# Performance work log

Hardware: AMD Instinct MI355X
Metric: run time of the kernel (lower is better)

The kernel has to match this reference:

```python
import jax, jax.numpy as jnp
import numpy as np

HID = 192
EPS = 1e-5

def _bn(x, g, b):
    # BatchNorm1d, training mode: batch stats over all leading axes, biased var
    ax = tuple(range(x.ndim - 1))
    m = x.mean(axis=ax)
    v = x.var(axis=ax)
    return (x - m) * jax.lax.rsqrt(v + EPS) * g + b

def _glorot(k, shape):
    lim = np.sqrt(6.0 / (shape[0] + shape[1]))
    return jax.random.uniform(k, shape, jnp.float32, -lim, lim)

def setup_inputs() -> dict:
    key = jax.random.key(0)
    ks = jax.random.split(key, 8)
    B, N, F, C = 16, 1024, 128, 10
    x = jax.random.normal(ks[0], (B, N, F), jnp.float32)
    adj = (jax.random.uniform(ks[1], (B, N, N)) < 0.01).astype(jnp.float32)
    adj = jnp.maximum(adj, jnp.swapaxes(adj, 1, 2))
    return dict(
        x=x, adj=adj,
        bn_feat_g=jnp.ones((F,), jnp.float32), bn_feat_b=jnp.full((F,), 1e-4, jnp.float32),
        W_feat=_glorot(ks[2], (F, HID)),
        bns_conv_g=jnp.ones((3, HID), jnp.float32), bns_conv_b=jnp.full((3, HID), 1e-4, jnp.float32),
        convs_W=jnp.stack([_glorot(jax.random.fold_in(ks[3], i), (HID, HID)) for i in range(3)]),
        convs_b=jnp.zeros((3, HID), jnp.float32),
        bn_fc_g=jnp.ones((HID,), jnp.float32), bn_fc_b=jnp.full((HID,), 1e-4, jnp.float32),
        lin_W=_glorot(ks[4], (HID, HID)), lin_b=jnp.zeros((HID,), jnp.float32),
        bn_hid_g=jnp.ones((HID,), jnp.float32), bn_hid_b=jnp.full((HID,), 1e-4, jnp.float32),
        cls_W=_glorot(ks[5], (HID, 10)), cls_b=jnp.zeros((10,), jnp.float32),
    )

def reference(x, adj, bn_feat_g, bn_feat_b, W_feat, bns_conv_g, bns_conv_b,
              convs_W, convs_b, bn_fc_g, bn_fc_b, lin_W, lin_b,
              bn_hid_g, bn_hid_b, cls_W, cls_b):
    B, N, _ = x.shape
    # dense_to_sparse discards edge values -> binary edges; add remaining self loops (weight 1)
    A = (adj != 0).astype(x.dtype)
    A = jnp.maximum(A, jnp.eye(N, dtype=x.dtype))
    deg = A.sum(-1)                                   # [B,N]
    dis = jnp.where(deg > 0, deg ** -0.5, 0.0)
    A_hat = dis[:, :, None] * A * dis[:, None, :]      # D^-1/2 (A+I) D^-1/2
    h = _bn(x, bn_feat_g, bn_feat_b)
    # conv_feat has gfn=True: pure linear transform, no bias, no propagation
    h = jax.nn.relu(jnp.einsum('bnf,fh->bnh', h, W_feat))
    for i in range(convs_W.shape[0]):
        h = _bn(h, bns_conv_g[i], bns_conv_b[i])
        h = jax.nn.relu(jnp.einsum('bij,bjh->bih', A_hat, h @ convs_W[i]) + convs_b[i])
    g = h.mean(axis=1)                                 # global_mean_pool -> [B,HID]
    g = _bn(g, bn_fc_g, bn_fc_b)
    g = jax.nn.relu(g @ lin_W + lin_b)
    g = _bn(g, bn_hid_g, bn_hid_b)
    logits = g @ cls_W + cls_b
    return jax.nn.log_softmax(logits, axis=-1)
```

## Files before the change

### kernel.cpp

```cpp
#include <hip/hip_runtime.h>
#include <hip/hip_bf16.h>

#define BB 16
#define NN 1024
#define FF 128
#define HH 192
#define NROWS (BB*NN)
#define MAXC 128
#define EPSV 1e-5f

constexpr size_t OFF_H0  = 0;
constexpr size_t OFF_ZB  = OFF_H0 + (size_t)NROWS*HH/2;
constexpr size_t OFF_WPF = OFF_ZB + (size_t)NROWS*HH/2;
constexpr size_t OFF_WPC = OFF_WPF + (size_t)HH*FF/2;
constexpr size_t OFF_BF  = OFF_WPC + (size_t)HH*HH/2;
constexpr size_t OFF_BC  = OFF_BF + HH;
constexpr size_t OFF_DIS = OFF_BC + HH;
constexpr size_t OFF_G   = OFF_DIS + NROWS;
constexpr size_t OFF_ST  = OFF_G + BB*HH;
constexpr size_t ST_SIZE = 512 + 3*8*512;
constexpr size_t OFF_FLAG= OFF_ST + ST_SIZE;
constexpr size_t OFF_CNT = OFF_FLAG + 1;
constexpr size_t OFF_COLS= OFF_CNT + NROWS;

typedef __attribute__((ext_vector_type(8))) short short8;
typedef __attribute__((ext_vector_type(4))) float f32x4;
typedef __attribute__((ext_vector_type(4))) unsigned int u32x4;
typedef __attribute__((ext_vector_type(2))) unsigned int u32x2;

static __device__ __forceinline__ float bf(const __hip_bfloat16 v) {
    return __bfloat162float(v);
}
static __device__ __forceinline__ float ldin(const void* p, size_t i, int isf) {
    return isf ? ((const float*)p)[i]
               : __bfloat162float(((const __hip_bfloat16*)p)[i]);
}
static __host__ __device__ __forceinline__ float* stage_h(float* ws, int s ) {
    return ws + OFF_ST + 512 + (size_t)s*8*512;
}
static __device__ __forceinline__ float blo(unsigned int u) {
    union { unsigned int x; float f; } v; v.x = u << 16; return v.f;
}
static __device__ __forceinline__ float bhi(unsigned int u) {
    union { unsigned int x; float f; } v; v.x = u & 0xFFFF0000u; return v.f;
}
static __device__ __forceinline__ unsigned int packbf(float a, float b) {
    union { unsigned int u; __hip_bfloat16 h[2]; } p;
    p.h[0] = __float2bfloat16(a); p.h[1] = __float2bfloat16(b);
    return p.u;
}

__global__ void detect_and_zero(const unsigned int* __restrict__ adjw, float* ws) {
    __shared__ int evid;
    int tid = threadIdx.x;
    if (tid == 0) evid = 0;
    __syncthreads();
    int local = 0;
    for (int k = tid; k < 16384; k += 256) {
        unsigned int w = adjw[k];
        if ((w & 0xFFFFu) == 0x3F80u) local++;
    }
    if (local) atomicAdd(&evid, local);
    for (size_t k = tid; k < ST_SIZE; k += 256) ws[OFF_ST + k] = 0.f;
    for (int k = tid; k < BB*HH; k += 256) ws[OFF_G + k] = 0.f;
    __syncthreads();
    if (tid == 0) ((int*)ws)[OFF_FLAG] = (evid == 0) ? 1 : 0;
}

__global__ __launch_bounds__(256) void phase1(const void* __restrict__ adj,
                                              const void* __restrict__ x, float* ws) {
    const int isf = ((const int*)ws)[OFF_FLAG];
    int tid = threadIdx.x;
    if (blockIdx.x < NROWS) {
        int row = blockIdx.x;
        int i   = row & (NN - 1);
        __shared__ int cnt_s;
        __shared__ unsigned short colbuf[MAXC];
        if (tid == 0) cnt_s = 0;
        __syncthreads();
        int j0 = tid*4;
        unsigned int bits[4];
        if (isf) {
            u32x4 v = *(const u32x4*)((const unsigned int*)adj + (size_t)row*NN + j0);
            bits[0]=v[0]; bits[1]=v[1]; bits[2]=v[2]; bits[3]=v[3];
        } else {
            u32x2 v = *(const u32x2*)((const unsigned short*)adj + (size_t)row*NN + j0);
            bits[0]=(v[0]&0xFFFFu); bits[1]=(v[0]>>16); bits[2]=(v[1]&0xFFFFu); bits[3]=(v[1]>>16);
        }
        #pragma unroll
        for (int e = 0; e < 4; ++e) {
            int j = j0 + e;
            if ((bits[e] << 1) != 0u || j == i) {
                int p = atomicAdd(&cnt_s, 1);
                if (p < MAXC) colbuf[p] = (unsigned short)j;
            }
        }
        __syncthreads();
        int c = cnt_s; if (c > MAXC) c = MAXC;
        if (tid == 0) {
            ((int*)(ws + OFF_CNT))[row] = c;
            ws[OFF_DIS + row] = rsqrtf((float)cnt_s);
        }
        unsigned short* cols = (unsigned short*)(ws + OFF_COLS);
        for (int k = tid; k < c; k += 256) cols[(size_t)row*MAXC + k] = colbuf[k];
    } else {
        int b2 = blockIdx.x - NROWS;
        int f = tid & (FF-1), half = tid >> 7;
        int r0 = b2*64 + half*32;
        float s = 0.f, sq = 0.f;
        for (int r = 0; r < 32; ++r) {
            float v = ldin(x, (size_t)(r0 + r)*FF + f, isf);
            s += v; sq += v*v;
        }
        atomicAdd(&ws[OFF_ST + f], s);
        atomicAdd(&ws[OFF_ST + 256 + f], sq);
    }
}

__global__ void prep_feat(const void* __restrict__ W_feat,
                          const void* __restrict__ gg, const void* __restrict__ bb,
                          float* ws) {
    const int isf = ((const int*)ws)[OFF_FLAG];
    int n = blockIdx.x, k = threadIdx.x;
    const float* st = ws + OFF_ST;
    float m   = st[k] * (1.f/NROWS);
    float var = st[256+k] * (1.f/NROWS) - m*m;
    float a   = ldin(gg, k, isf) * rsqrtf(var + EPSV);
    float c   = ldin(bb, k, isf) - m*a;
    float wv  = ldin(W_feat, (size_t)k*HH + n, isf);
    ((__hip_bfloat16*)(ws + OFF_WPF))[(size_t)n*FF + k] = __float2bfloat16(a*wv);
    __shared__ float red[FF];
    red[k] = c*wv;
    __syncthreads();
    for (int s = FF/2; s > 0; s >>= 1) {
        if (k < s) red[k] += red[k + s];
        __syncthreads();
    }
    if (k == 0) ws[OFF_BF + n] = red[0];
}

__global__ void prep_conv(const void* __restrict__ convs_W,
                          const void* __restrict__ gg, const void* __restrict__ bb,
                          int layer, float* ws) {
    const int isf = ((const int*)ws)[OFF_FLAG];
    int n = blockIdx.x, k = threadIdx.x;
    const float* st = stage_h(ws, layer);
    float s = 0.f, sq = 0.f;
    #pragma unroll
    for (int bkt = 0; bkt < 8; ++bkt) {
        s  += st[bkt*512 + k];
        sq += st[bkt*512 + 256 + k];
    }
    float m   = s * (1.f/NROWS);
    float var = sq * (1.f/NROWS) - m*m;
    float a   = ldin(gg, (size_t)layer*HH + k, isf) * rsqrtf(var + EPSV);
    float c   = ldin(bb, (size_t)layer*HH + k, isf) - m*a;
    float wv  = ldin(convs_W, (size_t)layer*HH*HH + (size_t)k*HH + n, isf);
    ((__hip_bfloat16*)(ws + OFF_WPC))[(size_t)n*HH + k] = __float2bfloat16(a*wv);
    __shared__ float red[HH];
    red[k] = c*wv;
    __syncthreads();
    if (k < 96) red[k] += red[k + 96];
    __syncthreads();
    for (int s2 = 48; s2 >= 3; s2 >>= 1) {
        if (k < s2) red[k] += red[k + s2];
        __syncthreads();
    }
    if (k == 0) ws[OFF_BC + n] = red[0] + red[1] + red[2];
}

template<int K, int MODE>
__global__ __launch_bounds__(256) void gemm_mfma(const void* __restrict__ A,
                                                 const __hip_bfloat16* __restrict__ BT,
                                                 const float* __restrict__ bias,
                                                 float* __restrict__ ws) {
    const int isf = ((const int*)ws)[OFF_FLAG];
    int lane = threadIdx.x & 63, w = threadIdx.x >> 6;
    int wr = w & 1, wc = w >> 1;
    int bi = blockIdx.x;
    int batch = bi & 15, seg = bi >> 4;
    int row0 = batch*NN + seg*32 + wr*16;
    int col0 = wc*96;
    int m    = lane & 15, quad = lane >> 4;
    f32x4 acc[6];
    #pragma unroll
    for (int t = 0; t < 6; ++t) acc[t] = f32x4{0.f,0.f,0.f,0.f};
    float bv[6];
    #pragma unroll
    for (int t = 0; t < 6; ++t) bv[t] = bias[col0 + t*16 + m];
    #pragma unroll
    for (int kb = 0; kb < K/32; ++kb) {
        short8 a;
        if (MODE == 0 && isf) {
            const float* Ar = (const float*)A + (size_t)(row0+m)*K + kb*32 + quad*8;
            f32x4 v0 = *(const f32x4*)Ar;
            f32x4 v1 = *(const f32x4*)(Ar + 4);
            union { short8 s8; __hip_bfloat16 h[8]; } u;
            #pragma unroll
            for (int e = 0; e < 4; ++e) {
                u.h[e]   = __float2bfloat16(v0[e]);
                u.h[e+4] = __float2bfloat16(v1[e]);
            }
            a = u.s8;
        } else {
            a = *(const short8*)((const __hip_bfloat16*)A +
                                 (size_t)(row0+m)*K + kb*32 + quad*8);
        }
        #pragma unroll
        for (int t = 0; t < 6; ++t) {
            short8 b = *(const short8*)(BT + (size_t)(col0 + t*16+m)*K + kb*32 + quad*8);
            acc[t] = __builtin_amdgcn_mfma_f32_16x16x32_bf16(a, b, acc[t], 0, 0, 0);
        }
    }
    if (MODE == 0) {
        __shared__ float sh[2*HH];
        for (int i = threadIdx.x; i < 2*HH; i += 256) sh[i] = 0.f;
        __syncthreads();
        __hip_bfloat16* H0 = (__hip_bfloat16*)(ws + OFF_H0);
        #pragma unroll
        for (int t = 0; t < 6; ++t) {
            int ch = col0 + t*16 + m;
            float s = 0.f, sq = 0.f;
            #pragma unroll
            for (int r = 0; r < 4; ++r) {
                float o = fmaxf(acc[t][r] + bv[t], 0.f);
                H0[(size_t)(row0 + quad*4 + r)*HH + ch] = __float2bfloat16(o);
                s += o; sq += o*o;
            }
            atomicAdd(&sh[ch], s);
            atomicAdd(&sh[HH + ch], sq);
        }
        __syncthreads();
        float* st = stage_h(ws, 0) + (bi & 7)*512;
        if (threadIdx.x < HH) {
            atomicAdd(&st[threadIdx.x], sh[threadIdx.x]);
            atomicAdd(&st[256 + threadIdx.x], sh[HH + threadIdx.x]);
        }
    } else {
        const float* dis = ws + OFF_DIS;
        __hip_bfloat16* Z = (__hip_bfloat16*)(ws + OFF_ZB);
        float sc[4];
        #pragma unroll
        for (int r = 0; r < 4; ++r) sc[r] = dis[row0 + quad*4 + r];
        #pragma unroll
        for (int t = 0; t < 6; ++t)
            #pragma unroll
            for (int r = 0; r < 4; ++r)
                Z[(size_t)(row0 + quad*4 + r)*HH + col0 + t*16 + m] =
                    __float2bfloat16((acc[t][r] + bv[t]) * sc[r]);
    }
}

__global__ __launch_bounds__(512) void spmm(const void* __restrict__ bias, int layer,
                                            float* __restrict__ stat_out, int is_pool,
                                            float* ws) {
    __shared__ unsigned int Zs[NN*16];
    const int isf = ((const int*)ws)[OFF_FLAG];
    int tid = threadIdx.x;
    int bi = blockIdx.x;
    int batch = bi & 15;
    int rest  = bi >> 4;
    int slice = rest % 6;
    int half  = rest / 6;
    int c0 = slice*32;
    const unsigned int* Zu = (const unsigned int*)(ws + OFF_ZB)
                             + (size_t)batch*NN*96 + c0/2;
    for (int i = tid; i < NN*16; i += 512) {
        int r = i >> 4, u = i & 15;
        Zs[i] = Zu[(size_t)r*96 + u];
    }
    __syncthreads();
    int d = tid & 7, rslot = tid >> 3;
    const float* dis = ws + OFF_DIS;
    const int* cnt = (const int*)(ws + OFF_CNT);
    const unsigned short* cols = (const unsigned short*)(ws + OFF_COLS);
    unsigned int* H0u = (unsigned int*)(ws + OFF_H0);
    float bch[4];
    #pragma unroll
    for (int e = 0; e < 4; ++e)
        bch[e] = ldin(bias, (size_t)layer*HH + c0 + d*4 + e, isf);
    float s_acc[4] = {0.f,0.f,0.f,0.f}, q_acc[4] = {0.f,0.f,0.f,0.f};
    for (int it = 0; it < 8; ++it) {
        int row = batch*NN + half*512 + it*64 + rslot;
        int c = cnt[row];
        const unsigned short* cl = cols + (size_t)row*MAXC;
        float a0=0.f, a1=0.f, a2=0.f, a3=0.f;
        int k = 0;
        for (; k + 8 <= c; k += 8) {
            u32x4 cw = *(const u32x4*)(cl + k);
            int j[8];
            j[0]=(int)(cw[0]&0xFFFFu); j[1]=(int)(cw[0]>>16);
            j[2]=(int)(cw[1]&0xFFFFu); j[3]=(int)(cw[1]>>16);
            j[4]=(int)(cw[2]&0xFFFFu); j[5]=(int)(cw[2]>>16);
            j[6]=(int)(cw[3]&0xFFFFu); j[7]=(int)(cw[3]>>16);
            u32x2 z[8];
            #pragma unroll
            for (int e = 0; e < 8; ++e)
                z[e] = *(const u32x2*)(&Zs[j[e]*16 + d*2]);
            #pragma unroll
            for (int e = 0; e < 8; ++e) {
                a0 += blo(z[e][0]); a1 += bhi(z[e][0]);
                a2 += blo(z[e][1]); a3 += bhi(z[e][1]);
            }
        }
        for (; k < c; ++k) {
            u32x2 z = *(const u32x2*)(&Zs[(int)cl[k]*16 + d*2]);
            a0 += blo(z[0]); a1 += bhi(z[0]);
            a2 += blo(z[1]); a3 += bhi(z[1]);
        }
        float dd = dis[row];
        float o0 = fmaxf(dd*a0 + bch[0], 0.f);
        float o1 = fmaxf(dd*a1 + bch[1], 0.f);
        float o2 = fmaxf(dd*a2 + bch[2], 0.f);
        float o3 = fmaxf(dd*a3 + bch[3], 0.f);
        u32x2 outw; outw[0] = packbf(o0,o1); outw[1] = packbf(o2,o3);
        *(u32x2*)(&H0u[(size_t)row*96 + c0/2 + d*2]) = outw;
        s_acc[0]+=o0; s_acc[1]+=o1; s_acc[2]+=o2; s_acc[3]+=o3;
        q_acc[0]+=o0*o0; q_acc[1]+=o1*o1; q_acc[2]+=o2*o2; q_acc[3]+=o3*o3;
    }
    #pragma unroll
    for (int e = 0; e < 4; ++e) {
        #pragma unroll
        for (int mask = 8; mask < 64; mask <<= 1) {
            s_acc[e] += __shfl_xor(s_acc[e], mask, 64);
            q_acc[e] += __shfl_xor(q_acc[e], mask, 64);
        }
    }
    if ((tid & 63) < 8) {
        if (is_pool) {
            #pragma unroll
            for (int e = 0; e < 4; ++e)
                atomicAdd(&ws[OFF_G + (size_t)batch*HH + c0 + d*4 + e], s_acc[e]);
        } else {
            float* st = stat_out + (bi & 7)*512;
            #pragma unroll
            for (int e = 0; e < 4; ++e) {
                atomicAdd(&st[c0 + d*4 + e],       s_acc[e]);
                atomicAdd(&st[256 + c0 + d*4 + e], q_acc[e]);
            }
        }
    }
}

__global__ __launch_bounds__(768) void tail(
                     const void* __restrict__ fc_g,  const void* __restrict__ fc_b,
                     const void* __restrict__ lin_W, const void* __restrict__ lin_b,
                     const void* __restrict__ hid_g, const void* __restrict__ hid_b,
                     const void* __restrict__ cls_W, const void* __restrict__ cls_b,
                     void* __restrict__ out, const float* ws) {
    __shared__ float g1[BB][HH];
    __shared__ float g2[BB][HH];
    __shared__ __hip_bfloat16 Wl[HH*HH];
    __shared__ float logits[BB][10];
    __shared__ float lse[BB];
    int tid = threadIdx.x;
    const int isf = ((const int*)ws)[OFF_FLAG];
    const float* g = ws + OFF_G;
    if (isf) {
        const float* Wp = (const float*)lin_W;
        for (int i = tid; i < HH*HH; i += 768) Wl[i] = __float2bfloat16(Wp[i]);
    } else {
        const __hip_bfloat16* Wp = (const __hip_bfloat16*)lin_W;
        for (int i = tid; i < HH*HH; i += 768) Wl[i] = Wp[i];
    }
    if (tid < HH) {
        float s = 0.f, sq = 0.f;
        for (int b = 0; b < BB; ++b) {
            float v = g[b*HH + tid] * (1.f/NN);
            s += v; sq += v*v;
        }
        float m = s*(1.f/BB), var = sq*(1.f/BB) - m*m;
        float a = ldin(fc_g, tid, isf) * rsqrtf(var + EPSV);
        float c = ldin(fc_b, tid, isf) - m*a;
        for (int b = 0; b < BB; ++b) g1[b][tid] = g[b*HH + tid]*(1.f/NN)*a + c;
    }
    __syncthreads();
    {
        int n = tid % HH, bg = tid / HH;
        float lb = ldin(lin_b, n, isf);
        float a0 = lb, a1 = lb, a2 = lb, a3 = lb;
        int b0 = bg*4;
        for (int k = 0; k < HH; ++k) {
            float wv = bf(Wl[k*HH + n]);
            a0 += g1[b0+0][k]*wv;
            a1 += g1[b0+1][k]*wv;
            a2 += g1[b0+2][k]*wv;
            a3 += g1[b0+3][k]*wv;
        }
        g2[b0+0][n] = fmaxf(a0, 0.f);
        g2[b0+1][n] = fmaxf(a1, 0.f);
        g2[b0+2][n] = fmaxf(a2, 0.f);
        g2[b0+3][n] = fmaxf(a3, 0.f);
    }
    __syncthreads();
    if (tid < HH) {
        float s = 0.f, sq = 0.f;
        for (int b = 0; b < BB; ++b) { float v = g2[b][tid]; s += v; sq += v*v; }
        float m = s*(1.f/BB), var = sq*(1.f/BB) - m*m;
        float a = ldin(hid_g, tid, isf) * rsqrtf(var + EPSV);
        float c = ldin(hid_b, tid, isf) - m*a;
        for (int b = 0; b < BB; ++b) g2[b][tid] = g2[b][tid]*a + c;
    }
    __syncthreads();
    if (tid < BB*10) {
        int b = tid/10, k = tid%10;
        float acc = ldin(cls_b, k, isf);
        for (int h = 0; h < HH; ++h) acc += g2[b][h] * ldin(cls_W, (size_t)h*10 + k, isf);
        logits[b][k] = acc;
    }
    __syncthreads();
    if (tid < BB) {
        float m = -1e30f;
        for (int k = 0; k < 10; ++k) m = fmaxf(m, logits[tid][k]);
        float s = 0.f;
        for (int k = 0; k < 10; ++k) s += expf(logits[tid][k] - m);
        lse[tid] = m + logf(s);
    }
    __syncthreads();
    if (tid < BB*10) {
        int b = tid/10;
        float v = logits[b][tid%10] - lse[b];
        if (isf) ((float*)out)[tid] = v;
        else     ((__hip_bfloat16*)out)[tid] = __float2bfloat16(v);
    }
}

extern "C" void kernel_launch(void* const* d_in, const int* in_sizes, int n_in,
                              void* d_out, int out_size, void* d_ws, size_t ws_size,
                              hipStream_t stream) {
    const void* x       = d_in[0];
    const void* adj     = d_in[1];
    const void* bnf_g   = d_in[2];
    const void* bnf_b   = d_in[3];
    const void* W_feat  = d_in[4];
    const void* bnc_g   = d_in[5];
    const void* bnc_b   = d_in[6];
    const void* convs_W = d_in[7];
    const void* convs_b = d_in[8];
    const void* fc_g    = d_in[9];
    const void* fc_b    = d_in[10];
    const void* lin_W   = d_in[11];
    const void* lin_b   = d_in[12];
    const void* hid_g   = d_in[13];
    const void* hid_b   = d_in[14];
    const void* cls_W   = d_in[15];
    const void* cls_b   = d_in[16];

    float* ws = (float*)d_ws;
    const __hip_bfloat16* WPF = (const __hip_bfloat16*)(ws + OFF_WPF);
    const __hip_bfloat16* WPC = (const __hip_bfloat16*)(ws + OFF_WPC);

    detect_and_zero<<<1, 256, 0, stream>>>((const unsigned int*)adj, ws);
    phase1<<<NROWS + 256, 256, 0, stream>>>(adj, x, ws);
    prep_feat<<<HH, FF, 0, stream>>>(W_feat, bnf_g, bnf_b, ws);
    gemm_mfma<FF, 0><<<NROWS/32, 256, 0, stream>>>(x, WPF, ws + OFF_BF, ws);
    for (int l = 0; l < 3; ++l) {
        prep_conv<<<HH, HH, 0, stream>>>(convs_W, bnc_g, bnc_b, l, ws);
        gemm_mfma<HH, 1><<<NROWS/32, 256, 0, stream>>>(
            (const void*)(ws + OFF_H0), WPC, ws + OFF_BC, ws);
        spmm<<<192, 512, 0, stream>>>(convs_b, l,
            (l < 2) ? stage_h(ws, l + 1) : nullptr, (l == 2) ? 1 : 0, ws);
    }
    tail<<<1, 768, 0, stream>>>(fc_g, fc_b, lin_W, lin_b,
                                hid_g, hid_b, cls_W, cls_b, d_out, ws);
}
```

Before: 331.7 us.

## Fuse pipeline into one cooperative persistent kernel with grid syncs

Replaces the chain of about a dozen kernel launches with a single cooperative kernel of 256 blocks that runs init, graph build, BN-folded weight prep, GEMMs and SpMM, separated by grid.sync. Work is repartitioned so each block handles 64 adjacency rows, two 32-row GEMM tiles, and a 24-column SpMM slice. The aim is to remove launch and inter-kernel gaps. In exchange, the graph phase now uses 256 blocks instead of 16k, grid-wide barriers are added, and there is a multi-kernel fallback if the cooperative launch fails.

Result: slower. 1.163 ms (+250.7%).

```diff
diff --git a/kernel.cpp b/kernel.cpp
--- a/kernel.cpp
+++ b/kernel.cpp
@@ -1,5 +1,7 @@
 #include <hip/hip_runtime.h>
 #include <hip/hip_bf16.h>
+#include <hip/hip_cooperative_groups.h>
+namespace cg = cooperative_groups;
 
 #define BB 16
 #define NN 1024
@@ -8,6 +10,8 @@
 #define NROWS (BB*NN)
 #define MAXC 128
 #define EPSV 1e-5f
+#define NBLK 256
+#define SMEM_BYTES (NN*12*4)
 
 constexpr size_t OFF_H0  = 0;
 constexpr size_t OFF_ZB  = OFF_H0 + (size_t)NROWS*HH/2;
@@ -18,7 +22,7 @@
 constexpr size_t OFF_DIS = OFF_BC + HH;
 constexpr size_t OFF_G   = OFF_DIS + NROWS;
 constexpr size_t OFF_ST  = OFF_G + BB*HH;
-constexpr size_t ST_SIZE = 512 + 3*8*512;
+constexpr size_t ST_SIZE = 4*8*512;
 constexpr size_t OFF_FLAG= OFF_ST + ST_SIZE;
 constexpr size_t OFF_CNT = OFF_FLAG + 1;
 constexpr size_t OFF_COLS= OFF_CNT + NROWS;
@@ -35,8 +39,8 @@
     return isf ? ((const float*)p)[i]
                : __bfloat162float(((const __hip_bfloat16*)p)[i]);
 }
-static __host__ __device__ __forceinline__ float* stage_h(float* ws, int s ) {
-    return ws + OFF_ST + 512 + (size_t)s*8*512;
+static __host__ __device__ __forceinline__ float* stage_hh(float* ws, int s ) {
+    return ws + OFF_ST + (size_t)8*512*(1 + s);
 }
 static __device__ __forceinline__ float blo(unsigned int u) {
     union { unsigned int x; float f; } v; v.x = u << 16; return v.f;
@@ -50,148 +54,161 @@
     return p.u;
 }
 
-__global__ void detect_and_zero(const unsigned int* __restrict__ adjw, float* ws) {
-    __shared__ int evid;
-    int tid = threadIdx.x;
-    if (tid == 0) evid = 0;
-    __syncthreads();
-    int local = 0;
-    for (int k = tid; k < 16384; k += 256) {
-        unsigned int w = adjw[k];
-        if ((w & 0xFFFFu) == 0x3F80u) local++;
-    }
-    if (local) atomicAdd(&evid, local);
-    for (size_t k = tid; k < ST_SIZE; k += 256) ws[OFF_ST + k] = 0.f;
-    for (int k = tid; k < BB*HH; k += 256) ws[OFF_G + k] = 0.f;
-    __syncthreads();
-    if (tid == 0) ((int*)ws)[OFF_FLAG] = (evid == 0) ? 1 : 0;
-}
-
-__global__ __launch_bounds__(256) void phase1(const void* __restrict__ adj,
-                                              const void* __restrict__ x, float* ws) {
-    const int isf = ((const int*)ws)[OFF_FLAG];
-    int tid = threadIdx.x;
-    if (blockIdx.x < NROWS) {
-        int row = blockIdx.x;
-        int i   = row & (NN - 1);
-        __shared__ int cnt_s;
-        __shared__ unsigned short colbuf[MAXC];
-        if (tid == 0) cnt_s = 0;
-        __syncthreads();
-        int j0 = tid*4;
-        unsigned int bits[4];
-        if (isf) {
-            u32x4 v = *(const u32x4*)((const unsigned int*)adj + (size_t)row*NN + j0);
-            bits[0]=v[0]; bits[1]=v[1]; bits[2]=v[2]; bits[3]=v[3];
-        } else {
-            u32x2 v = *(const u32x2*)((const unsigned short*)adj + (size_t)row*NN + j0);
-            bits[0]=(v[0]&0xFFFFu); bits[1]=(v[0]>>16); bits[2]=(v[1]&0xFFFFu); bits[3]=(v[1]>>16);
-        }
-        #pragma unroll
-        for (int e = 0; e < 4; ++e) {
-            int j = j0 + e;
-            if ((bits[e] << 1) != 0u || j == i) {
-                int p = atomicAdd(&cnt_s, 1);
-                if (p < MAXC) colbuf[p] = (unsigned short)j;
+
+static __device__ void init_body(const unsigned int* __restrict__ adjw, float* ws,
+                                 int bi, int tid, int* evid) {
+    if (bi == 0) {
+        if (tid == 0) *evid = 0;
+        __syncthreads();
+        int local = 0;
+        for (int k = tid; k < 16384; k += 256)
+            if ((adjw[k] & 0xFFFFu) == 0x3F80u) local++;
+        if (local) atomicAdd(evid, local);
+        __syncthreads();
+        if (tid == 0) ((int*)ws)[OFF_FLAG] = (*evid == 0) ? 1 : 0;
+    }
+    size_t ztot = BB*HH + ST_SIZE;
+    for (size_t i = (size_t)bi*256 + tid; i < ztot; i += (size_t)NBLK*256)
+        ws[OFF_G + i] = 0.f;
+}
+
+static __device__ void graph_body(const void* __restrict__ adj,
+                                  const void* __restrict__ x, float* ws,
+                                  int isf, int bi, int tid, unsigned char* smem) {
+    int* cnt_s = (int*)smem;
+    unsigned short* colbuf = (unsigned short*)(smem + 16);
+    int* cntg = (int*)(ws + OFF_CNT);
+    unsigned short* colsg = (unsigned short*)(ws + OFF_COLS);
+    int r4 = tid >> 6, tl = tid & 63;
+    for (int rr = 0; rr < 16; ++rr) {
+        int row = bi*64 + rr*4 + r4;
+        int i = row & (NN - 1);
+        if (tl == 0) cnt_s[r4] = 0;
+        __syncthreads();
+        #pragma unroll
+        for (int p = 0; p < 4; ++p) {
+            int j0 = p*256 + tl*4;
+            unsigned int bits[4];
+            if (isf) {
+                u32x4 v = *(const u32x4*)((const unsigned int*)adj + (size_t)row*NN + j0);
+                bits[0]=v[0]; bits[1]=v[1]; bits[2]=v[2]; bits[3]=v[3];
+            } else {
+                u32x2 v = *(const u32x2*)((const unsigned short*)adj + (size_t)row*NN + j0);
+                bits[0]=(v[0]&0xFFFFu); bits[1]=(v[0]>>16);
+                bits[2]=(v[1]&0xFFFFu); bits[3]=(v[1]>>16);
             }
-        }
-        __syncthreads();
-        int c = cnt_s; if (c > MAXC) c = MAXC;
-        if (tid == 0) {
-            ((int*)(ws + OFF_CNT))[row] = c;
-            ws[OFF_DIS + row] = rsqrtf((float)cnt_s);
-        }
-        unsigned short* cols = (unsigned short*)(ws + OFF_COLS);
-        for (int k = tid; k < c; k += 256) cols[(size_t)row*MAXC + k] = colbuf[k];
-    } else {
-        int b2 = blockIdx.x - NROWS;
-        int f = tid & (FF-1), half = tid >> 7;
-        int r0 = b2*64 + half*32;
-        float s = 0.f, sq = 0.f;
-        for (int r = 0; r < 32; ++r) {
-            float v = ldin(x, (size_t)(r0 + r)*FF + f, isf);
-            s += v; sq += v*v;
-        }
-        atomicAdd(&ws[OFF_ST + f], s);
-        atomicAdd(&ws[OFF_ST + 256 + f], sq);
-    }
-}
-
-__global__ void prep_feat(const void* __restrict__ W_feat,
-                          const void* __restrict__ gg, const void* __restrict__ bb,
-                          float* ws) {
-    const int isf = ((const int*)ws)[OFF_FLAG];
-    int n = blockIdx.x, k = threadIdx.x;
-    const float* st = ws + OFF_ST;
-    float m   = st[k] * (1.f/NROWS);
-    float var = st[256+k] * (1.f/NROWS) - m*m;
-    float a   = ldin(gg, k, isf) * rsqrtf(var + EPSV);
-    float c   = ldin(bb, k, isf) - m*a;
-    float wv  = ldin(W_feat, (size_t)k*HH + n, isf);
-    ((__hip_bfloat16*)(ws + OFF_WPF))[(size_t)n*FF + k] = __float2bfloat16(a*wv);
-    __shared__ float red[FF];
-    red[k] = c*wv;
-    __syncthreads();
-    for (int s = FF/2; s > 0; s >>= 1) {
-        if (k < s) red[k] += red[k + s];
-        __syncthreads();
-    }
-    if (k == 0) ws[OFF_BF + n] = red[0];
-}
-
-__global__ void prep_conv(const void* __restrict__ convs_W,
-                          const void* __restrict__ gg, const void* __restrict__ bb,
-                          int layer, float* ws) {
-    const int isf = ((const int*)ws)[OFF_FLAG];
-    int n = blockIdx.x, k = threadIdx.x;
-    const float* st = stage_h(ws, layer);
-    float s = 0.f, sq = 0.f;
-    #pragma unroll
-    for (int bkt = 0; bkt < 8; ++bkt) {
-        s  += st[bkt*512 + k];
-        sq += st[bkt*512 + 256 + k];
-    }
-    float m   = s * (1.f/NROWS);
-    float var = sq * (1.f/NROWS) - m*m;
-    float a   = ldin(gg, (size_t)layer*HH + k, isf) * rsqrtf(var + EPSV);
-    float c   = ldin(bb, (size_t)layer*HH + k, isf) - m*a;
-    float wv  = ldin(convs_W, (size_t)layer*HH*HH + (size_t)k*HH + n, isf);
-    ((__hip_bfloat16*)(ws + OFF_WPC))[(size_t)n*HH + k] = __float2bfloat16(a*wv);
-    __shared__ float red[HH];
-    red[k] = c*wv;
-    __syncthreads();
-    if (k < 96) red[k] += red[k + 96];
+            #pragma unroll
+            for (int e = 0; e < 4; ++e) {
+                int j = j0 + e;
+                if ((bits[e] << 1) != 0u || j == i) {
+                    int p2 = atomicAdd(&cnt_s[r4], 1);
+                    if (p2 < MAXC) colbuf[r4*MAXC + p2] = (unsigned short)j;
+                }
+            }
+        }
+        __syncthreads();
+        int c = cnt_s[r4]; if (c > MAXC) c = MAXC;
+        if (tl == 0) {
+            cntg[row] = c;
+            ws[OFF_DIS + row] = rsqrtf((float)cnt_s[r4]);
+        }
+        for (int k = tl; k < c; k += 64) colsg[(size_t)row*MAXC + k] = colbuf[r4*MAXC + k];
+        __syncthreads();
+    }
+    float* xs = (float*)smem;
+    int f = tid & 127, rr2 = tid >> 7;
+    float s = 0.f, q = 0.f;
+    int r0 = bi*64;
+    for (int r = rr2; r < 64; r += 2) {
+        float v = ldin(x, (size_t)(r0 + r)*FF + f, isf);
+        s += v; q += v*v;
+    }
+    __syncthreads();
+    if (rr2 == 1) { xs[f] = s; xs[128 + f] = q; }
+    __syncthreads();
+    if (rr2 == 0) {
+        s += xs[f]; q += xs[128 + f];
+        float* st = ws + OFF_ST + (size_t)(bi & 7)*512;
+        atomicAdd(&st[f], s);
+        atomicAdd(&st[256 + f], q);
+    }
+    __syncthreads();
+}
+
+static __device__ void prep_feat_body(const void* __restrict__ W_feat,
+                                      const void* __restrict__ gg, const void* __restrict__ bb,
+                                      float* ws, int isf, int n, int tid, float* red) {
+    int k = tid;
+    if (k < FF) {
+        const float* st = ws + OFF_ST;
+        float s = 0.f, q = 0.f;
+        #pragma unroll
+        for (int b = 0; b < 8; ++b) { s += st[b*512 + k]; q += st[b*512 + 256 + k]; }
+        float mm = s * (1.f/NROWS);
+        float var = q * (1.f/NROWS) - mm*mm;
+        float a = ldin(gg, k, isf) * rsqrtf(var + EPSV);
+        float cc = ldin(bb, k, isf) - mm*a;
+        float wv = ldin(W_feat, (size_t)k*HH + n, isf);
+        ((__hip_bfloat16*)(ws + OFF_WPF))[(size_t)n*FF + k] = __float2bfloat16(a*wv);
+        red[k] = cc*wv;
+    }
+    __syncthreads();
+    for (int s2 = 64; s2 > 0; s2 >>= 1) {
+        if (tid < s2 && tid + s2 < FF) red[tid] += red[tid + s2];
+        __syncthreads();
+    }
+    if (tid == 0) ws[OFF_BF + n] = red[0];
+    __syncthreads();
+}
+
+static __device__ void prep_conv_body(const void* __restrict__ convs_W,
+                                      const void* __restrict__ gg, const void* __restrict__ bb,
+                                      int l, float* ws, int isf, int n, int tid, float* red) {
+    int k = tid;
+    if (k < HH) {
+        const float* st = stage_hh(ws, l);
+        float s = 0.f, q = 0.f;
+        #pragma unroll
+        for (int b = 0; b < 8; ++b) { s += st[b*512 + k]; q += st[b*512 + 256 + k]; }
+        float mm = s * (1.f/NROWS);
+        float var = q * (1.f/NROWS) - mm*mm;
+        float a = ldin(gg, (size_t)l*HH + k, isf) * rsqrtf(var + EPSV);
+        float cc = ldin(bb, (size_t)l*HH + k, isf) - mm*a;
+        float wv = ldin(convs_W, (size_t)l*HH*HH + (size_t)k*HH + n, isf);
+        ((__hip_bfloat16*)(ws + OFF_WPC))[(size_t)n*HH + k] = __float2bfloat16(a*wv);
+        red[k] = cc*wv;
+    }
+    __syncthreads();
+    if (tid < 96) red[tid] += red[tid + 96];
     __syncthreads();
     for (int s2 = 48; s2 >= 3; s2 >>= 1) {
-        if (k < s2) red[k] += red[k + s2];
-        __syncthreads();
-    }
-    if (k == 0) ws[OFF_BC + n] = red[0] + red[1] + red[2];
-}
-
-template<int K, int MODE>
-__global__ __launch_bounds__(256) void gemm_mfma(const void* __restrict__ A,
-                                                 const __hip_bfloat16* __restrict__ BT,
-                                                 const float* __restrict__ bias,
-                                                 float* __restrict__ ws) {
-    const int isf = ((const int*)ws)[OFF_FLAG];
-    int lane = threadIdx.x & 63, w = threadIdx.x >> 6;
+        if (tid < s2) red[tid] += red[tid + s2];
+        __syncthreads();
+    }
+    if (tid == 0) ws[OFF_BC + n] = red[0] + red[1] + red[2];
+    __syncthreads();
+}
+
+static __device__ void gemm_body(int K, int mode, const void* __restrict__ A,
+                                 const __hip_bfloat16* __restrict__ BT,
+                                 const float* __restrict__ bias,
+                                 int isf, int bi, int half, int tid,
+                                 float* __restrict__ ws, unsigned char* smem) {
+    int lane = tid & 63, w = tid >> 6;
     int wr = w & 1, wc = w >> 1;
-    int bi = blockIdx.x;
     int batch = bi & 15, seg = bi >> 4;
-    int row0 = batch*NN + seg*32 + wr*16;
+    int row0 = batch*NN + seg*64 + half*32 + wr*16;
     int col0 = wc*96;
-    int m    = lane & 15, quad = lane >> 4;
+    int m = lane & 15, quad = lane >> 4;
     f32x4 acc[6];
     #pragma unroll
     for (int t = 0; t < 6; ++t) acc[t] = f32x4{0.f,0.f,0.f,0.f};
     float bv[6];
     #pragma unroll
     for (int t = 0; t < 6; ++t) bv[t] = bias[col0 + t*16 + m];
-    #pragma unroll
     for (int kb = 0; kb < K/32; ++kb) {
         short8 a;
-        if (MODE == 0 && isf) {
+        if (mode == 0 && isf) {
             const float* Ar = (const float*)A + (size_t)(row0+m)*K + kb*32 + quad*8;
             f32x4 v0 = *(const f32x4*)Ar;
             f32x4 v1 = *(const f32x4*)(Ar + 4);
@@ -212,9 +229,9 @@
             acc[t] = __builtin_amdgcn_mfma_f32_16x16x32_bf16(a, b, acc[t], 0, 0, 0);
         }
     }
-    if (MODE == 0) {
-        __shared__ float sh[2*HH];
-        for (int i = threadIdx.x; i < 2*HH; i += 256) sh[i] = 0.f;
+    if (mode == 0) {
+        float* sh = (float*)smem;
+        for (int i = tid; i < 2*HH; i += 256) sh[i] = 0.f;
         __syncthreads();
         __hip_bfloat16* H0 = (__hip_bfloat16*)(ws + OFF_H0);
         #pragma unroll
@@ -231,11 +248,12 @@
             atomicAdd(&sh[HH + ch], sq);
         }
         __syncthreads();
-        float* st = stage_h(ws, 0) + (bi & 7)*512;
-        if (threadIdx.x < HH) {
-            atomicAdd(&st[threadIdx.x], sh[threadIdx.x]);
-            atomicAdd(&st[256 + threadIdx.x], sh[HH + threadIdx.x]);
-        }
+        float* st = stage_hh(ws, 0) + (size_t)(bi & 7)*512;
+        if (tid < HH) {
+            atomicAdd(&st[tid], sh[tid]);
+            atomicAdd(&st[256 + tid], sh[HH + tid]);
+        }
+        __syncthreads();
     } else {
         const float* dis = ws + OFF_DIS;
         __hip_bfloat16* Z = (__hip_bfloat16*)(ws + OFF_ZB);
@@ -251,95 +269,187 @@
     }
 }
 
-__global__ __launch_bounds__(512) void spmm(const void* __restrict__ bias, int layer,
-                                            float* __restrict__ stat_out, int is_pool,
-                                            float* ws) {
-    __shared__ unsigned int Zs[NN*16];
-    const int isf = ((const int*)ws)[OFF_FLAG];
-    int tid = threadIdx.x;
-    int bi = blockIdx.x;
+static __device__ void spmm_body(int l, const void* __restrict__ convs_b,
+                                 int isf, int bi, int tid,
+                                 float* __restrict__ ws, unsigned char* smem) {
+    unsigned int* Zs = (unsigned int*)smem;
     int batch = bi & 15;
     int rest  = bi >> 4;
-    int slice = rest % 6;
-    int half  = rest / 6;
-    int c0 = slice*32;
+    int slice = rest & 7;
+    int rgrp  = rest >> 3;
+    int c0 = slice*24;
     const unsigned int* Zu = (const unsigned int*)(ws + OFF_ZB)
-                             + (size_t)batch*NN*96 + c0/2;
-    for (int i = tid; i < NN*16; i += 512) {
-        int r = i >> 4, u = i & 15;
+                             + (size_t)batch*NN*96 + slice*12;
+    for (int i = tid; i < NN*12; i += 256) {
+        int r = i / 12, u = i - r*12;
         Zs[i] = Zu[(size_t)r*96 + u];
     }
     __syncthreads();
-    int d = tid & 7, rslot = tid >> 3;
+    int d = tid & 3, rslot = tid >> 2;
     const float* dis = ws + OFF_DIS;
     const int* cnt = (const int*)(ws + OFF_CNT);
     const unsigned short* cols = (const unsigned short*)(ws + OFF_COLS);
     unsigned int* H0u = (unsigned int*)(ws + OFF_H0);
-    float bch[4];
+    float bch[6];
     #pragma unroll
-    for (int e = 0; e < 4; ++e)
-        bch[e] = ldin(bias, (size_t)layer*HH + c0 + d*4 + e, isf);
-    float s_acc[4] = {0.f,0.f,0.f,0.f}, q_acc[4] = {0.f,0.f,0.f,0.f};
+    for (int e = 0; e < 6; ++e)
+        bch[e] = ldin(convs_b, (size_t)l*HH + c0 + d*6 + e, isf);
+    float s_acc[6] = {0,0,0,0,0,0}, q_acc[6] = {0,0,0,0,0,0};
     for (int it = 0; it < 8; ++it) {
-        int row = batch*NN + half*512 + it*64 + rslot;
+        int row = batch*NN + rgrp*512 + it*64 + rslot;
         int c = cnt[row];
         const unsigned short* cl = cols + (size_t)row*MAXC;
-        float a0=0.f, a1=0.f, a2=0.f, a3=0.f;
+        float a[6] = {0,0,0,0,0,0};
         int k = 0;
-        for (; k + 8 <= c; k += 8) {
-            u32x4 cw = *(const u32x4*)(cl + k);
-            int j[8];
-            j[0]=(int)(cw[0]&0xFFFFu); j[1]=(int)(cw[0]>>16);
-            j[2]=(int)(cw[1]&0xFFFFu); j[3]=(int)(cw[1]>>16);
-            j[4]=(int)(cw[2]&0xFFFFu); j[5]=(int)(cw[2]>>16);
-            j[6]=(int)(cw[3]&0xFFFFu); j[7]=(int)(cw[3]>>16);
-            u32x2 z[8];
-            #pragma unroll
-            for (int e = 0; e < 8; ++e)
-                z[e] = *(const u32x2*)(&Zs[j[e]*16 + d*2]);
-            #pragma unroll
-            for (int e = 0; e < 8; ++e) {
-                a0 += blo(z[e][0]); a1 += bhi(z[e][0]);
-                a2 += blo(z[e][1]); a3 += bhi(z[e][1]);
+        for (; k + 4 <= c; k += 4) {
+            u32x2 cw = *(const u32x2*)(cl + k);
+            int j0=(int)(cw[0]&0xFFFFu), j1=(int)(cw[0]>>16);
+            int j2=(int)(cw[1]&0xFFFFu), j3=(int)(cw[1]>>16);
+            int o0=j0*12+d*3, o1=j1*12+d*3, o2=j2*12+d*3, o3=j3*12+d*3;
+            unsigned int z[12];
+            z[0]=Zs[o0]; z[1]=Zs[o0+1]; z[2]=Zs[o0+2];
+            z[3]=Zs[o1]; z[4]=Zs[o1+1]; z[5]=Zs[o1+2];
+            z[6]=Zs[o2]; z[7]=Zs[o2+1]; z[8]=Zs[o2+2];
+            z[9]=Zs[o3]; z[10]=Zs[o3+1]; z[11]=Zs[o3+2];
+            #pragma unroll
+            for (int g = 0; g < 4; ++g) {
+                a[0]+=blo(z[g*3]);   a[1]+=bhi(z[g*3]);
+                a[2]+=blo(z[g*3+1]); a[3]+=bhi(z[g*3+1]);
+                a[4]+=blo(z[g*3+2]); a[5]+=bhi(z[g*3+2]);
             }
         }
         for (; k < c; ++k) {
-            u32x2 z = *(const u32x2*)(&Zs[(int)cl[k]*16 + d*2]);
-            a0 += blo(z[0]); a1 += bhi(z[0]);
-            a2 += blo(z[1]); a3 += bhi(z[1]);
+            int o = (int)cl[k]*12 + d*3;
+            unsigned int z0=Zs[o], z1=Zs[o+1], z2=Zs[o+2];
+            a[0]+=blo(z0); a[1]+=bhi(z0);
+            a[2]+=blo(z1); a[3]+=bhi(z1);
+            a[4]+=blo(z2); a[5]+=bhi(z2);
         }
         float dd = dis[row];
-        float o0 = fmaxf(dd*a0 + bch[0], 0.f);
-        float o1 = fmaxf(dd*a1 + bch[1], 0.f);
-        float o2 = fmaxf(dd*a2 + bch[2], 0.f);
-        float o3 = fmaxf(dd*a3 + bch[3], 0.f);
-        u32x2 outw; outw[0] = packbf(o0,o1); outw[1] = packbf(o2,o3);
-        *(u32x2*)(&H0u[(size_t)row*96 + c0/2 + d*2]) = outw;
-        s_acc[0]+=o0; s_acc[1]+=o1; s_acc[2]+=o2; s_acc[3]+=o3;
-        q_acc[0]+=o0*o0; q_acc[1]+=o1*o1; q_acc[2]+=o2*o2; q_acc[3]+=o3*o3;
+        float o0 = fmaxf(dd*a[0] + bch[0], 0.f);
+        float o1 = fmaxf(dd*a[1] + bch[1], 0.f);
+        float o2 = fmaxf(dd*a[2] + bch[2], 0.f);
+        float o3 = fmaxf(dd*a[3] + bch[3], 0.f);
+        float o4 = fmaxf(dd*a[4] + bch[4], 0.f);
+        float o5 = fmaxf(dd*a[5] + bch[5], 0.f);
+        size_t hb = (size_t)row*96 + slice*12 + d*3;
+        H0u[hb]   = packbf(o0,o1);
+        H0u[hb+1] = packbf(o2,o3);
+        H0u[hb+2] = packbf(o4,o5);
+        s_acc[0]+=o0; s_acc[1]+=o1; s_acc[2]+=o2; s_acc[3]+=o3; s_acc[4]+=o4; s_acc[5]+=o5;
+        q_acc[0]+=o0*o0; q_acc[1]+=o1*o1; q_acc[2]+=o2*o2;
+        q_acc[3]+=o3*o3; q_acc[4]+=o4*o4; q_acc[5]+=o5*o5;
     }
     #pragma unroll
-    for (int e = 0; e < 4; ++e) {
-        #pragma unroll
-        for (int mask = 8; mask < 64; mask <<= 1) {
+    for (int e = 0; e < 6; ++e) {
+        #pragma unroll
+        for (int mask = 4; mask < 64; mask <<= 1) {
             s_acc[e] += __shfl_xor(s_acc[e], mask, 64);
             q_acc[e] += __shfl_xor(q_acc[e], mask, 64);
         }
     }
-    if ((tid & 63) < 8) {
-        if (is_pool) {
-            #pragma unroll
-            for (int e = 0; e < 4; ++e)
-                atomicAdd(&ws[OFF_G + (size_t)batch*HH + c0 + d*4 + e], s_acc[e]);
+    if ((tid & 63) < 4) {
+        if (l == 2) {
+            #pragma unroll
+            for (int e = 0; e < 6; ++e)
+                atomicAdd(&ws[OFF_G + (size_t)batch*HH + c0 + d*6 + e], s_acc[e]);
         } else {
-            float* st = stat_out + (bi & 7)*512;
-            #pragma unroll
-            for (int e = 0; e < 4; ++e) {
-                atomicAdd(&st[c0 + d*4 + e],       s_acc[e]);
-                atomicAdd(&st[256 + c0 + d*4 + e], q_acc[e]);
+            float* st = stage_hh(ws, l + 1) + (size_t)(bi & 7)*512;
+            #pragma unroll
+            for (int e = 0; e < 6; ++e) {
+                atomicAdd(&st[c0 + d*6 + e],       s_acc[e]);
+                atomicAdd(&st[256 + c0 + d*6 + e], q_acc[e]);
             }
         }
     }
+    __syncthreads();
+}
+
+__global__ __launch_bounds__(256) void mega(const void* __restrict__ x,
+        const void* __restrict__ adj,
+        const void* __restrict__ bnf_g, const void* __restrict__ bnf_b,
+        const void* __restrict__ W_feat,
+        const void* __restrict__ bnc_g, const void* __restrict__ bnc_b,
+        const void* __restrict__ convs_W, const void* __restrict__ convs_b,
+        float* __restrict__ ws) {
+    cg::grid_group grid = cg::this_grid();
+    __shared__ __align__(16) unsigned char smem[SMEM_BYTES];
+    int tid = threadIdx.x, bi = blockIdx.x;
+
+    init_body((const unsigned int*)adj, ws, bi, tid, (int*)smem);
+    __threadfence(); grid.sync(); __threadfence();
+
+    const int isf = ((const int*)ws)[OFF_FLAG];
+
+    graph_body(adj, x, ws, isf, bi, tid, smem);
+    __threadfence(); grid.sync(); __threadfence();
+
+    if (bi < HH) prep_feat_body(W_feat, bnf_g, bnf_b, ws, isf, bi, tid, (float*)smem);
+    __threadfence(); grid.sync(); __threadfence();
+
+    for (int half = 0; half < 2; ++half)
+        gemm_body(FF, 0, x, (const __hip_bfloat16*)(ws + OFF_WPF), ws + OFF_BF,
+                  isf, bi, half, tid, ws, smem);
+    __threadfence(); grid.sync(); __threadfence();
+
+    for (int l = 0; l < 3; ++l) {
+        if (bi < HH) prep_conv_body(convs_W, bnc_g, bnc_b, l, ws, isf, bi, tid, (float*)smem);
+        __threadfence(); grid.sync(); __threadfence();
+
+        for (int half = 0; half < 2; ++half)
+            gemm_body(HH, 1, (const void*)(ws + OFF_H0),
+                      (const __hip_bfloat16*)(ws + OFF_WPC), ws + OFF_BC,
+                      isf, bi, half, tid, ws, smem);
+        __threadfence(); grid.sync(); __threadfence();
+
+        spmm_body(l, convs_b, isf, bi, tid, ws, smem);
+        if (l < 2) { __threadfence(); grid.sync(); __threadfence(); }
+    }
+}
+
+__global__ __launch_bounds__(256) void k_init(const unsigned int* __restrict__ adjw,
+                                              float* ws) {
+    __shared__ int evid;
+    init_body(adjw, ws, blockIdx.x, threadIdx.x, &evid);
+}
+__global__ __launch_bounds__(256) void k_graph(const void* __restrict__ adj,
+                                               const void* __restrict__ x, float* ws) {
+    __shared__ __align__(16) unsigned char sm[2048];
+    const int isf = ((const int*)ws)[OFF_FLAG];
+    graph_body(adj, x, ws, isf, blockIdx.x, threadIdx.x, sm);
+}
+__global__ __launch_bounds__(256) void k_prep_feat(const void* __restrict__ W_feat,
+        const void* __restrict__ gg, const void* __restrict__ bb, float* ws) {
+    __shared__ float red[FF];
+    const int isf = ((const int*)ws)[OFF_FLAG];
+    prep_feat_body(W_feat, gg, bb, ws, isf, blockIdx.x, threadIdx.x, red);
+}
+__global__ __launch_bounds__(256) void k_prep_conv(const void* __restrict__ convs_W,
+        const void* __restrict__ gg, const void* __restrict__ bb, int l, float* ws) {
+    __shared__ float red[HH];
+    const int isf = ((const int*)ws)[OFF_FLAG];
+    prep_conv_body(convs_W, gg, bb, l, ws, isf, blockIdx.x, threadIdx.x, red);
+}
+__global__ __launch_bounds__(256) void k_gemm_feat(const void* __restrict__ x, float* ws) {
+    __shared__ __align__(16) unsigned char sm[2*HH*4];
+    const int isf = ((const int*)ws)[OFF_FLAG];
+    for (int half = 0; half < 2; ++half)
+        gemm_body(FF, 0, x, (const __hip_bfloat16*)(ws + OFF_WPF), ws + OFF_BF,
+                  isf, blockIdx.x, half, threadIdx.x, ws, sm);
+}
+__global__ __launch_bounds__(256) void k_gemm_conv(int l, float* ws) {
+    const int isf = ((const int*)ws)[OFF_FLAG];
+    for (int half = 0; half < 2; ++half)
+        gemm_body(HH, 1, (const void*)(ws + OFF_H0),
+                  (const __hip_bfloat16*)(ws + OFF_WPC), ws + OFF_BC,
+                  isf, blockIdx.x, half, threadIdx.x, ws, nullptr);
+    (void)l;
+}
+__global__ __launch_bounds__(256) void k_spmm(const void* __restrict__ convs_b,
+                                              int l, float* ws) {
+    __shared__ __align__(16) unsigned char sm[SMEM_BYTES];
+    const int isf = ((const int*)ws)[OFF_FLAG];
+    spmm_body(l, convs_b, isf, blockIdx.x, threadIdx.x, ws, sm);
 }
 
 __global__ __launch_bounds__(768) void tail(
@@ -447,19 +557,23 @@
     const void* cls_b   = d_in[16];
 
     float* ws = (float*)d_ws;
-    const __hip_bfloat16* WPF = (const __hip_bfloat16*)(ws + OFF_WPF);
-    const __hip_bfloat16* WPC = (const __hip_bfloat16*)(ws + OFF_WPC);
-
-    detect_and_zero<<<1, 256, 0, stream>>>((const unsigned int*)adj, ws);
-    phase1<<<NROWS + 256, 256, 0, stream>>>(adj, x, ws);
-    prep_feat<<<HH, FF, 0, stream>>>(W_feat, bnf_g, bnf_b, ws);
-    gemm_mfma<FF, 0><<<NROWS/32, 256, 0, stream>>>(x, WPF, ws + OFF_BF, ws);
-    for (int l = 0; l < 3; ++l) {
-        prep_conv<<<HH, HH, 0, stream>>>(convs_W, bnc_g, bnc_b, l, ws);
-        gemm_mfma<HH, 1><<<NROWS/32, 256, 0, stream>>>(
-            (const void*)(ws + OFF_H0), WPC, ws + OFF_BC, ws);
-        spmm<<<192, 512, 0, stream>>>(convs_b, l,
-            (l < 2) ? stage_h(ws, l + 1) : nullptr, (l == 2) ? 1 : 0, ws);
+
+    void* args[] = {(void*)&x, (void*)&adj, (void*)&bnf_g, (void*)&bnf_b,
+                    (void*)&W_feat, (void*)&bnc_g, (void*)&bnc_b,
+                    (void*)&convs_W, (void*)&convs_b, (void*)&ws};
+    hipError_t cerr = hipLaunchCooperativeKernel(reinterpret_cast<void*>(mega),
+                                                 dim3(NBLK), dim3(256), args, 0, stream);
+    if (cerr != hipSuccess) {
+        (void)hipGetLastError();
+        k_init<<<NBLK, 256, 0, stream>>>((const unsigned int*)adj, ws);
+        k_graph<<<NBLK, 256, 0, stream>>>(adj, x, ws);
+        k_prep_feat<<<HH, 256, 0, stream>>>(W_feat, bnf_g, bnf_b, ws);
+        k_gemm_feat<<<NBLK, 256, 0, stream>>>(x, ws);
+        for (int l = 0; l < 3; ++l) {
+            k_prep_conv<<<HH, 256, 0, stream>>>(convs_W, bnc_g, bnc_b, l, ws);
+            k_gemm_conv<<<NBLK, 256, 0, stream>>>(l, ws);
+            k_spmm<<<NBLK, 256, 0, stream>>>(convs_b, l, ws);
+        }
     }
     tail<<<1, 768, 0, stream>>>(fc_g, fc_b, lin_W, lin_b,
                                 hid_g, hid_b, cls_W, cls_b, d_out, ws);
```

## Fold BN weight-prep kernels into preceding kernels via last-block tickets

Applied to the files above, without the earlier changes.

Removes the separate prep_feat and prep_conv launches. The producing kernels (phase1, gemm_mfma MODE 0, spmm) each take an atomic ticket, and the last block to finish reads the accumulated BatchNorm statistics. That block then builds the scaled bf16 weight matrix and folded bias for the next layer. This is meant to cut kernel-launch and inter-kernel idle gaps. In exchange, the weight folding runs serially in a single block with shared-memory atomics, which may lengthen the critical path.

New measurement: 953.4 us. 187% more time.

```diff
diff --git a/kernel.cpp b/kernel.cpp
--- a/kernel.cpp
+++ b/kernel.cpp
@@ -20,7 +20,8 @@
 constexpr size_t OFF_ST  = OFF_G + BB*HH;
 constexpr size_t ST_SIZE = 512 + 3*8*512;
 constexpr size_t OFF_FLAG= OFF_ST + ST_SIZE;
-constexpr size_t OFF_CNT = OFF_FLAG + 1;
+constexpr size_t OFF_TICK= OFF_FLAG + 1;
+constexpr size_t OFF_CNT = OFF_TICK + 4;
 constexpr size_t OFF_COLS= OFF_CNT + NROWS;
 
 typedef __attribute__((ext_vector_type(8))) short short8;
@@ -38,6 +39,9 @@
 static __host__ __device__ __forceinline__ float* stage_h(float* ws, int s ) {
     return ws + OFF_ST + 512 + (size_t)s*8*512;
 }
+static __device__ __forceinline__ float aread(float* p) {
+    return atomicAdd(p, 0.0f);
+}
 static __device__ __forceinline__ float blo(unsigned int u) {
     union { unsigned int x; float f; } v; v.x = u << 16; return v.f;
 }
@@ -61,14 +65,18 @@
         if ((w & 0xFFFFu) == 0x3F80u) local++;
     }
     if (local) atomicAdd(&evid, local);
-    for (size_t k = tid; k < ST_SIZE; k += 256) ws[OFF_ST + k] = 0.f;
-    for (int k = tid; k < BB*HH; k += 256) ws[OFF_G + k] = 0.f;
+    size_t ztot = BB*HH + ST_SIZE + 1 + 4;
+    for (size_t k = tid; k < ztot; k += 256) ws[OFF_G + k] = 0.f;
     __syncthreads();
     if (tid == 0) ((int*)ws)[OFF_FLAG] = (evid == 0) ? 1 : 0;
 }
 
 __global__ __launch_bounds__(256) void phase1(const void* __restrict__ adj,
-                                              const void* __restrict__ x, float* ws) {
+                                              const void* __restrict__ x,
+                                              const void* __restrict__ W_feat,
+                                              const void* __restrict__ bnf_g,
+                                              const void* __restrict__ bnf_b,
+                                              float* ws) {
     const int isf = ((const int*)ws)[OFF_FLAG];
     int tid = threadIdx.x;
     if (blockIdx.x < NROWS) {
@@ -115,67 +123,45 @@
         atomicAdd(&ws[OFF_ST + f], s);
         atomicAdd(&ws[OFF_ST + 256 + f], sq);
     }
-}
-
-__global__ void prep_feat(const void* __restrict__ W_feat,
-                          const void* __restrict__ gg, const void* __restrict__ bb,
-                          float* ws) {
-    const int isf = ((const int*)ws)[OFF_FLAG];
-    int n = blockIdx.x, k = threadIdx.x;
-    const float* st = ws + OFF_ST;
-    float m   = st[k] * (1.f/NROWS);
-    float var = st[256+k] * (1.f/NROWS) - m*m;
-    float a   = ldin(gg, k, isf) * rsqrtf(var + EPSV);
-    float c   = ldin(bb, k, isf) - m*a;
-    float wv  = ldin(W_feat, (size_t)k*HH + n, isf);
-    ((__hip_bfloat16*)(ws + OFF_WPF))[(size_t)n*FF + k] = __float2bfloat16(a*wv);
-    __shared__ float red[FF];
-    red[k] = c*wv;
-    __syncthreads();
-    for (int s = FF/2; s > 0; s >>= 1) {
-        if (k < s) red[k] += red[k + s];
-        __syncthreads();
-    }
-    if (k == 0) ws[OFF_BF + n] = red[0];
-}
-
-__global__ void prep_conv(const void* __restrict__ convs_W,
-                          const void* __restrict__ gg, const void* __restrict__ bb,
-                          int layer, float* ws) {
-    const int isf = ((const int*)ws)[OFF_FLAG];
-    int n = blockIdx.x, k = threadIdx.x;
-    const float* st = stage_h(ws, layer);
-    float s = 0.f, sq = 0.f;
-    #pragma unroll
-    for (int bkt = 0; bkt < 8; ++bkt) {
-        s  += st[bkt*512 + k];
-        sq += st[bkt*512 + 256 + k];
-    }
-    float m   = s * (1.f/NROWS);
-    float var = sq * (1.f/NROWS) - m*m;
-    float a   = ldin(gg, (size_t)layer*HH + k, isf) * rsqrtf(var + EPSV);
-    float c   = ldin(bb, (size_t)layer*HH + k, isf) - m*a;
-    float wv  = ldin(convs_W, (size_t)layer*HH*HH + (size_t)k*HH + n, isf);
-    ((__hip_bfloat16*)(ws + OFF_WPC))[(size_t)n*HH + k] = __float2bfloat16(a*wv);
-    __shared__ float red[HH];
-    red[k] = c*wv;
-    __syncthreads();
-    if (k < 96) red[k] += red[k + 96];
-    __syncthreads();
-    for (int s2 = 48; s2 >= 3; s2 >>= 1) {
-        if (k < s2) red[k] += red[k + s2];
-        __syncthreads();
-    }
-    if (k == 0) ws[OFF_BC + n] = red[0] + red[1] + red[2];
+    __shared__ int tk;
+    __shared__ float fa[FF], fc[FF], fb[HH];
+    __syncthreads();
+    if (tid == 0) { __threadfence(); tk = atomicAdd(&((int*)ws)[OFF_TICK + 0], 1); }
+    __syncthreads();
+    if (tk != NROWS + 256 - 1) return;
+    if (tid < FF) {
+        float s = aread(&ws[OFF_ST + tid]);
+        float q = aread(&ws[OFF_ST + 256 + tid]);
+        float m = s * (1.f/NROWS);
+        float var = q * (1.f/NROWS) - m*m;
+        float a = ldin(bnf_g, tid, isf) * rsqrtf(var + EPSV);
+        fa[tid] = a;
+        fc[tid] = ldin(bnf_b, tid, isf) - m*a;
+    }
+    for (int i = tid; i < HH; i += 256) fb[i] = 0.f;
+    __syncthreads();
+    __hip_bfloat16* wpf = (__hip_bfloat16*)(ws + OFF_WPF);
+    for (int idx = tid; idx < HH*FF; idx += 256) {
+        int n = idx >> 7, k = idx & (FF-1);
+        float wv = ldin(W_feat, (size_t)k*HH + n, isf);
+        wpf[idx] = __float2bfloat16(fa[k]*wv);
+        atomicAdd(&fb[n], fc[k]*wv);
+    }
+    __syncthreads();
+    if (tid < HH) ws[OFF_BF + tid] = fb[tid];
 }
 
 template<int K, int MODE>
 __global__ __launch_bounds__(256) void gemm_mfma(const void* __restrict__ A,
                                                  const __hip_bfloat16* __restrict__ BT,
                                                  const float* __restrict__ bias,
+                                                 const void* __restrict__ convs_W,
+                                                 const void* __restrict__ bnc_g,
+                                                 const void* __restrict__ bnc_b,
                                                  float* __restrict__ ws) {
     const int isf = ((const int*)ws)[OFF_FLAG];
-    int lane = threadIdx.x & 63, w = threadIdx.x >> 6;
+    int tid = threadIdx.x;
+    int lane = tid & 63, w = tid >> 6;
     int wr = w & 1, wc = w >> 1;
     int bi = blockIdx.x;
     int batch = bi & 15, seg = bi >> 4;
@@ -214,7 +200,9 @@
     }
     if (MODE == 0) {
         __shared__ float sh[2*HH];
-        for (int i = threadIdx.x; i < 2*HH; i += 256) sh[i] = 0.f;
+        __shared__ float shb[HH];
+        __shared__ int tk;
+        for (int i = tid; i < 2*HH; i += 256) sh[i] = 0.f;
         __syncthreads();
         __hip_bfloat16* H0 = (__hip_bfloat16*)(ws + OFF_H0);
         #pragma unroll
@@ -231,11 +219,40 @@
             atomicAdd(&sh[HH + ch], sq);
         }
         __syncthreads();
-        float* st = stage_h(ws, 0) + (bi & 7)*512;
-        if (threadIdx.x < HH) {
-            atomicAdd(&st[threadIdx.x], sh[threadIdx.x]);
-            atomicAdd(&st[256 + threadIdx.x], sh[HH + threadIdx.x]);
-        }
+        float* st = stage_h(ws, 0) + (size_t)(bi & 7)*512;
+        if (tid < HH) {
+            atomicAdd(&st[tid], sh[tid]);
+            atomicAdd(&st[256 + tid], sh[HH + tid]);
+        }
+        __syncthreads();
+        if (tid == 0) { __threadfence(); tk = atomicAdd(&((int*)ws)[OFF_TICK + 1], 1); }
+        __syncthreads();
+        if (tk != NROWS/32 - 1) return;
+        if (tid < HH) {
+            float* s0 = stage_h(ws, 0);
+            float s = 0.f, q = 0.f;
+            #pragma unroll
+            for (int b = 0; b < 8; ++b) {
+                s += aread(&s0[b*512 + tid]);
+                q += aread(&s0[b*512 + 256 + tid]);
+            }
+            float mm = s * (1.f/NROWS);
+            float var = q * (1.f/NROWS) - mm*mm;
+            float a = ldin(bnc_g, tid, isf) * rsqrtf(var + EPSV);
+            sh[tid] = a;
+            sh[HH + tid] = ldin(bnc_b, tid, isf) - mm*a;
+        }
+        for (int i = tid; i < HH; i += 256) shb[i] = 0.f;
+        __syncthreads();
+        __hip_bfloat16* wpc = (__hip_bfloat16*)(ws + OFF_WPC);
+        for (int idx = tid; idx < HH*HH; idx += 256) {
+            int n = idx / HH, k = idx - n*HH;
+            float wv = ldin(convs_W, (size_t)k*HH + n, isf);
+            wpc[idx] = __float2bfloat16(sh[k]*wv);
+            atomicAdd(&shb[n], sh[HH + k]*wv);
+        }
+        __syncthreads();
+        if (tid < HH) ws[OFF_BC + tid] = shb[tid];
     } else {
         const float* dis = ws + OFF_DIS;
         __hip_bfloat16* Z = (__hip_bfloat16*)(ws + OFF_ZB);
@@ -253,8 +270,12 @@
 
 __global__ __launch_bounds__(512) void spmm(const void* __restrict__ bias, int layer,
                                             float* __restrict__ stat_out, int is_pool,
+                                            const void* __restrict__ convs_W,
+                                            const void* __restrict__ bnc_g,
+                                            const void* __restrict__ bnc_b,
                                             float* ws) {
     __shared__ unsigned int Zs[NN*16];
+    __shared__ int tk;
     const int isf = ((const int*)ws)[OFF_FLAG];
     int tid = threadIdx.x;
     int bi = blockIdx.x;
@@ -340,6 +361,40 @@
             }
         }
     }
+    if (is_pool) return;
+    __syncthreads();
+    if (tid == 0) { __threadfence(); tk = atomicAdd(&((int*)ws)[OFF_TICK + 2 + layer], 1); }
+    __syncthreads();
+    if (tk != 192 - 1) return;
+    float* fa = (float*)Zs;
+    float* fc = fa + HH;
+    float* fb = fa + 2*HH;
+    int l1 = layer + 1;
+    if (tid < HH) {
+        float* s0 = stat_out;
+        float s = 0.f, q = 0.f;
+        #pragma unroll
+        for (int b = 0; b < 8; ++b) {
+            s += aread(&s0[b*512 + tid]);
+            q += aread(&s0[b*512 + 256 + tid]);
+        }
+        float mm = s * (1.f/NROWS);
+        float var = q * (1.f/NROWS) - mm*mm;
+        float a = ldin(bnc_g, (size_t)l1*HH + tid, isf) * rsqrtf(var + EPSV);
+        fa[tid] = a;
+        fc[tid] = ldin(bnc_b, (size_t)l1*HH + tid, isf) - mm*a;
+    }
+    for (int i = tid; i < HH; i += 512) fb[i] = 0.f;
+    __syncthreads();
+    __hip_bfloat16* wpc = (__hip_bfloat16*)(ws + OFF_WPC);
+    for (int idx = tid; idx < HH*HH; idx += 512) {
+        int n = idx / HH, k = idx - n*HH;
+        float wv = ldin(convs_W, (size_t)l1*HH*HH + (size_t)k*HH + n, isf);
+        wpc[idx] = __float2bfloat16(fa[k]*wv);
+        atomicAdd(&fb[n], fc[k]*wv);
+    }
+    __syncthreads();
+    if (tid < HH) ws[OFF_BC + tid] = fb[tid];
 }
 
 __global__ __launch_bounds__(768) void tail(
@@ -451,15 +506,16 @@
     const __hip_bfloat16* WPC = (const __hip_bfloat16*)(ws + OFF_WPC);
 
     detect_and_zero<<<1, 256, 0, stream>>>((const unsigned int*)adj, ws);
-    phase1<<<NROWS + 256, 256, 0, stream>>>(adj, x, ws);
-    prep_feat<<<HH, FF, 0, stream>>>(W_feat, bnf_g, bnf_b, ws);
-    gemm_mfma<FF, 0><<<NROWS/32, 256, 0, stream>>>(x, WPF, ws + OFF_BF, ws);
+    phase1<<<NROWS + 256, 256, 0, stream>>>(adj, x, W_feat, bnf_g, bnf_b, ws);
+    gemm_mfma<FF, 0><<<NROWS/32, 256, 0, stream>>>(x, WPF, ws + OFF_BF,
+                                                   convs_W, bnc_g, bnc_b, ws);
     for (int l = 0; l < 3; ++l) {
-        prep_conv<<<HH, HH, 0, stream>>>(convs_W, bnc_g, bnc_b, l, ws);
         gemm_mfma<HH, 1><<<NROWS/32, 256, 0, stream>>>(
-            (const void*)(ws + OFF_H0), WPC, ws + OFF_BC, ws);
+            (const void*)(ws + OFF_H0), WPC, ws + OFF_BC,
+            convs_W, bnc_g, bnc_b, ws);
         spmm<<<192, 512, 0, stream>>>(convs_b, l,
-            (l < 2) ? stage_h(ws, l + 1) : nullptr, (l == 2) ? 1 : 0, ws);
+            (l < 2) ? stage_h(ws, l + 1) : nullptr, (l == 2) ? 1 : 0,
+            convs_W, bnc_g, bnc_b, ws);
     }
     tail<<<1, 768, 0, stream>>>(fc_g, fc_b, lin_W, lin_b,
                                 hid_g, hid_b, cls_W, cls_b, d_out, ws);
```
